# Optimization experiments

Hardware: AMD Instinct MI355X
Metric: run time of the kernel (lower is better)

Reference implementation:

```python
import jax, jax.numpy as jnp
import numpy as np

B, T, IN, H = 512, 512, 1, 64


def _lstm_dir(x, w_ih, w_hh, b_ih, b_hh, reverse):
    """Single-direction LSTM over x:[B,T,D]. PyTorch gate order i,f,g,o."""
    # Precompute input contribution for all timesteps (one big GEMM).
    xg = jnp.einsum('btd,gd->btg', x, w_ih) + (b_ih + b_hh)  # [B,T,4H]
    if reverse:
        xg = xg[:, ::-1]
    Hh = w_hh.shape[1]
    w_hh_t = w_hh.T  # [H,4H]

    def step(carry, g_t):
        h, c = carry
        g = g_t + h @ w_hh_t  # [B,4H]
        i, f, gc, o = jnp.split(g, 4, axis=-1)
        c = jax.nn.sigmoid(f) * c + jax.nn.sigmoid(i) * jnp.tanh(gc)
        h = jax.nn.sigmoid(o) * jnp.tanh(c)
        return (h, c), h

    b = x.shape[0]
    init = (jnp.zeros((b, Hh), x.dtype), jnp.zeros((b, Hh), x.dtype))
    _, hs = jax.lax.scan(step, init, jnp.swapaxes(xg, 0, 1))  # hs:[T,B,H]
    hs = jnp.swapaxes(hs, 0, 1)  # [B,T,H]
    return hs[:, ::-1] if reverse else hs


def _bilstm_layer(x, wf, rf, bf, bf2, wr, rr, br, br2):
    fwd = _lstm_dir(x, wf, rf, bf, bf2, reverse=False)
    bwd = _lstm_dir(x, wr, rr, br, br2, reverse=True)
    return jnp.concatenate([fwd, bwd], axis=-1)  # [B,T,2H]


def setup_inputs() -> dict:
    key = jax.random.key(0)
    ks = jax.random.split(key, 20)
    s = 1.0 / np.sqrt(H)
    u = lambda k, shape: jax.random.uniform(k, shape, jnp.float32, -s, s)
    inp = {'x': jax.random.normal(ks[0], (B, T, IN), jnp.float32)}
    # layer 0 (input dim IN), layer 1 (input dim 2H), fwd and reverse dirs
    inp['w_ih_l0'] = u(ks[1], (4 * H, IN)); inp['w_hh_l0'] = u(ks[2], (4 * H, H))
    inp['b_ih_l0'] = u(ks[3], (4 * H,));   inp['b_hh_l0'] = u(ks[4], (4 * H,))
    inp['w_ih_l0r'] = u(ks[5], (4 * H, IN)); inp['w_hh_l0r'] = u(ks[6], (4 * H, H))
    inp['b_ih_l0r'] = u(ks[7], (4 * H,));    inp['b_hh_l0r'] = u(ks[8], (4 * H,))
    inp['w_ih_l1'] = u(ks[9], (4 * H, 2 * H)); inp['w_hh_l1'] = u(ks[10], (4 * H, H))
    inp['b_ih_l1'] = u(ks[11], (4 * H,));      inp['b_hh_l1'] = u(ks[12], (4 * H,))
    inp['w_ih_l1r'] = u(ks[13], (4 * H, 2 * H)); inp['w_hh_l1r'] = u(ks[14], (4 * H, H))
    inp['b_ih_l1r'] = u(ks[15], (4 * H,));       inp['b_hh_l1r'] = u(ks[16], (4 * H,))
    inp['fc_w'] = u(ks[17], (1, 2 * H)); inp['fc_b'] = u(ks[18], (1,))
    return inp


def reference(x, w_ih_l0, w_hh_l0, b_ih_l0, b_hh_l0,
              w_ih_l0r, w_hh_l0r, b_ih_l0r, b_hh_l0r,
              w_ih_l1, w_hh_l1, b_ih_l1, b_hh_l1,
              w_ih_l1r, w_hh_l1r, b_ih_l1r, b_hh_l1r,
              fc_w, fc_b):
    h0 = _bilstm_layer(x, w_ih_l0, w_hh_l0, b_ih_l0, b_hh_l0,
                       w_ih_l0r, w_hh_l0r, b_ih_l0r, b_hh_l0r)
    h1 = _bilstm_layer(h0, w_ih_l1, w_hh_l1, b_ih_l1, b_hh_l1,
                       w_ih_l1r, w_hh_l1r, b_ih_l1r, b_hh_l1r)
    last = h1[:, -1, :]  # [B,2H]
    return last @ fc_w.T + fc_b  # [B,1]
```

## Files before the change

### kernel.cpp

```cpp
#include <hip/hip_runtime.h>
#include <cstddef>
#include <cstdint>

#define Tn 512
#define Bn 512

__device__ __forceinline__ float rlane(float v, int lane) {
    return __uint_as_float((unsigned)__builtin_amdgcn_readlane((int)__float_as_uint(v), lane));
}
__device__ __forceinline__ float sigm(float x) { return 1.0f / (1.0f + __expf(-x)); }
__device__ __forceinline__ float tanhf_(float x) { return 1.0f - 2.0f / (1.0f + __expf(2.0f * x)); }

#define BAR_LGKM() asm volatile("s_waitcnt lgkmcnt(0)\n\ts_barrier" ::: "memory")

__global__ __launch_bounds__(512, 2) void k_lstm_l0(
    const float* __restrict__ x,
    const float* __restrict__ wih_f, const float* __restrict__ whh_f,
    const float* __restrict__ bih_f, const float* __restrict__ bhh_f,
    const float* __restrict__ wih_r, const float* __restrict__ whh_r,
    const float* __restrict__ bih_r, const float* __restrict__ bhh_r,
    float* __restrict__ h0)
{
    const int tid = threadIdx.x;
    const int ti  = tid >> 7;
    const int kh  = (tid >> 6) & 1;
    const int j   = tid & 63;
    const int e   = ti >> 1;
    const int dir = ti & 1;
    const int b   = blockIdx.x * 2 + e;
    const int klo = kh * 32;

    const float* __restrict__ wih = dir ? wih_r : wih_f;
    const float* __restrict__ whh = dir ? whh_r : whh_f;
    const float* __restrict__ bih = dir ? bih_r : bih_f;
    const float* __restrict__ bhh = dir ? bhh_r : bhh_f;

    __shared__ float  xs[2][Tn];
    __shared__ float4 part[4][2][2][64];

    xs[0][tid] = x[(size_t)(blockIdx.x * 2 + 0) * Tn + tid];
    xs[1][tid] = x[(size_t)(blockIdx.x * 2 + 1) * Tn + tid];

    float wt[4][32];
    float wx[4], bias[4];
    #pragma unroll
    for (int g = 0; g < 4; ++g) {
        const int r = g * 64 + j;
        wx[g]   = wih[r];
        bias[g] = bih[r] + bhh[r];
        const float* __restrict__ ws = whh + (size_t)r * 64 + klo;
        #pragma unroll
        for (int k4 = 0; k4 < 8; ++k4) {
            const float4 w4 = *reinterpret_cast<const float4*>(ws + k4 * 4);
            wt[g][k4 * 4 + 0] = w4.x; wt[g][k4 * 4 + 1] = w4.y;
            wt[g][k4 * 4 + 2] = w4.z; wt[g][k4 * 4 + 3] = w4.w;
        }
    }
    __syncthreads();

    float h = 0.0f, c = 0.0f;
    float* __restrict__ outp = h0 + (size_t)b * Tn * 128 + dir * 64 + j;

    for (int s = 0; s < Tn; ++s) {
        const int t  = dir ? (Tn - 1 - s) : s;
        const int bf = s & 1;
        const float xt = xs[e][t];

        float a0 = 0.0f, a1 = 0.0f, a2 = 0.0f, a3 = 0.0f;
        #pragma unroll
        for (int kk = 0; kk < 32; ++kk) {
            const float hk = rlane(h, klo + kk);
            a0 = fmaf(hk, wt[0][kk], a0);
            a1 = fmaf(hk, wt[1][kk], a1);
            a2 = fmaf(hk, wt[2][kk], a2);
            a3 = fmaf(hk, wt[3][kk], a3);
        }
        part[ti][bf][kh][j] = make_float4(a0, a1, a2, a3);
        BAR_LGKM();
        const float4 pA = part[ti][bf][0][j];
        const float4 pB = part[ti][bf][1][j];
        const float gi = fmaf(xt, wx[0], bias[0]) + pA.x + pB.x;
        const float gf = fmaf(xt, wx[1], bias[1]) + pA.y + pB.y;
        const float gg = fmaf(xt, wx[2], bias[2]) + pA.z + pB.z;
        const float go = fmaf(xt, wx[3], bias[3]) + pA.w + pB.w;
        c = sigm(gf) * c + sigm(gi) * tanhf_(gg);
        h = sigm(go) * tanhf_(c);
        if (kh == 0) outp[(size_t)t * 128] = h;
    }
}

__global__ __launch_bounds__(512, 2) void k_lstm_l1f(
    const float* __restrict__ h0,
    const float* __restrict__ wih, const float* __restrict__ whh,
    const float* __restrict__ bih, const float* __restrict__ bhh,
    float* __restrict__ h1last)
{
    const int tid = threadIdx.x;
    const int e   = tid >> 8;
    const int wv  = (tid >> 6) & 3;
    const int j   = tid & 63;
    const int b   = blockIdx.x * 2 + e;
    const int kbase = wv * 48;

    __shared__ float4 part[2][2][4][64];

    float wt[4][48];
    float bias[4];
    #pragma unroll
    for (int g = 0; g < 4; ++g) {
        const int r = g * 64 + j;
        bias[g] = bih[r] + bhh[r];
        #pragma unroll
        for (int k4 = 0; k4 < 12; ++k4) {
            const int k = kbase + k4 * 4;
            const float* __restrict__ src = (k < 128)
                ? (wih + (size_t)r * 128 + k)
                : (whh + (size_t)r * 64 + (k - 128));
            const float4 w4 = *reinterpret_cast<const float4*>(src);
            wt[g][k4 * 4 + 0] = w4.x; wt[g][k4 * 4 + 1] = w4.y;
            wt[g][k4 * 4 + 2] = w4.z; wt[g][k4 * 4 + 3] = w4.w;
        }
    }

    const float* __restrict__ xrow = h0 + (size_t)b * Tn * 128;

    float x1a = 0.0f, x1b = 0.0f;
    if (wv <= 1) x1a = xrow[j];
    if (wv == 1 || wv == 2) x1b = xrow[64 + j];
    float h = 0.0f, c = 0.0f;

    for (int t = 0; t < Tn; ++t) {
        const int bf = t & 1;
        const int tn = (t + 1 < Tn) ? (t + 1) : t;
        float nx1a = 0.0f, nx1b = 0.0f;
        if (wv <= 1)            nx1a = xrow[(size_t)tn * 128 + j];
        if (wv == 1 || wv == 2) nx1b = xrow[(size_t)tn * 128 + 64 + j];

        float a0 = 0.0f, a1 = 0.0f, a2 = 0.0f, a3 = 0.0f;
        if (wv == 0) {
            #pragma unroll
            for (int kk = 0; kk < 48; ++kk) {
                const float v = rlane(x1a, kk);
                a0 = fmaf(v, wt[0][kk], a0); a1 = fmaf(v, wt[1][kk], a1);
                a2 = fmaf(v, wt[2][kk], a2); a3 = fmaf(v, wt[3][kk], a3);
            }
        } else if (wv == 1) {
            #pragma unroll
            for (int kk = 0; kk < 48; ++kk) {
                const float v = (kk < 16) ? rlane(x1a, 48 + kk) : rlane(x1b, kk - 16);
                a0 = fmaf(v, wt[0][kk], a0); a1 = fmaf(v, wt[1][kk], a1);
                a2 = fmaf(v, wt[2][kk], a2); a3 = fmaf(v, wt[3][kk], a3);
            }
        } else if (wv == 2) {
            #pragma unroll
            for (int kk = 0; kk < 48; ++kk) {
                const float v = (kk < 32) ? rlane(x1b, 32 + kk) : rlane(h, kk - 32);
                a0 = fmaf(v, wt[0][kk], a0); a1 = fmaf(v, wt[1][kk], a1);
                a2 = fmaf(v, wt[2][kk], a2); a3 = fmaf(v, wt[3][kk], a3);
            }
        } else {
            #pragma unroll
            for (int kk = 0; kk < 48; ++kk) {
                const float v = rlane(h, 16 + kk);
                a0 = fmaf(v, wt[0][kk], a0); a1 = fmaf(v, wt[1][kk], a1);
                a2 = fmaf(v, wt[2][kk], a2); a3 = fmaf(v, wt[3][kk], a3);
            }
        }
        part[e][bf][wv][j] = make_float4(a0, a1, a2, a3);
        BAR_LGKM();
        if (wv >= 2) {
            const float4 q0 = part[e][bf][0][j];
            const float4 q1 = part[e][bf][1][j];
            const float4 q2 = part[e][bf][2][j];
            const float4 q3 = part[e][bf][3][j];
            const float gi = bias[0] + q0.x + q1.x + q2.x + q3.x;
            const float gf = bias[1] + q0.y + q1.y + q2.y + q3.y;
            const float gg = bias[2] + q0.z + q1.z + q2.z + q3.z;
            const float go = bias[3] + q0.w + q1.w + q2.w + q3.w;
            c = sigm(gf) * c + sigm(gi) * tanhf_(gg);
            h = sigm(go) * tanhf_(c);
        }
        x1a = nx1a; x1b = nx1b;
    }
    if (wv == 2) h1last[(size_t)b * 64 + j] = h;
}

__global__ __launch_bounds__(64, 1) void k_l1r_fc(
    const float* __restrict__ h0,
    const float* __restrict__ wihr,
    const float* __restrict__ bihr, const float* __restrict__ bhhr,
    const float* __restrict__ h1last,
    const float* __restrict__ fcw, const float* __restrict__ fcb,
    float* __restrict__ out)
{
    const int b = blockIdx.x;
    const int j = threadIdx.x;
    const float* __restrict__ xrow = h0 + ((size_t)b * Tn + (Tn - 1)) * 128;
    const float x1a = xrow[j];
    const float x1b = xrow[64 + j];
    float acc[4];
    #pragma unroll
    for (int g = 0; g < 4; ++g) {
        const int r = g * 64 + j;
        float a = bihr[r] + bhhr[r];
        const float* __restrict__ wr = wihr + (size_t)r * 128;
        #pragma unroll
        for (int d4 = 0; d4 < 16; ++d4) {
            const float4 w4 = *reinterpret_cast<const float4*>(&wr[d4 * 4]);
            a = fmaf(rlane(x1a, d4 * 4 + 0), w4.x, a);
            a = fmaf(rlane(x1a, d4 * 4 + 1), w4.y, a);
            a = fmaf(rlane(x1a, d4 * 4 + 2), w4.z, a);
            a = fmaf(rlane(x1a, d4 * 4 + 3), w4.w, a);
        }
        #pragma unroll
        for (int d4 = 0; d4 < 16; ++d4) {
            const float4 w4 = *reinterpret_cast<const float4*>(&wr[64 + d4 * 4]);
            a = fmaf(rlane(x1b, d4 * 4 + 0), w4.x, a);
            a = fmaf(rlane(x1b, d4 * 4 + 1), w4.y, a);
            a = fmaf(rlane(x1b, d4 * 4 + 2), w4.z, a);
            a = fmaf(rlane(x1b, d4 * 4 + 3), w4.w, a);
        }
        acc[g] = a;
    }
    const float cr = sigm(acc[0]) * tanhf_(acc[2]);
    const float hr = sigm(acc[3]) * tanhf_(cr);
    float v = h1last[(size_t)b * 64 + j] * fcw[j] + hr * fcw[64 + j];
    #pragma unroll
    for (int off = 32; off > 0; off >>= 1) v += __shfl_xor(v, off, 64);
    if (j == 0) out[b] = v + fcb[0];
}

extern "C" void kernel_launch(void* const* d_in, const int* in_sizes, int n_in,
                              void* d_out, int out_size, void* d_ws, size_t ws_size,
                              hipStream_t stream)
{
    const float* x       = (const float*)d_in[0];
    const float* wih_l0  = (const float*)d_in[1];
    const float* whh_l0  = (const float*)d_in[2];
    const float* bih_l0  = (const float*)d_in[3];
    const float* bhh_l0  = (const float*)d_in[4];
    const float* wih_l0r = (const float*)d_in[5];
    const float* whh_l0r = (const float*)d_in[6];
    const float* bih_l0r = (const float*)d_in[7];
    const float* bhh_l0r = (const float*)d_in[8];
    const float* wih_l1  = (const float*)d_in[9];
    const float* whh_l1  = (const float*)d_in[10];
    const float* bih_l1  = (const float*)d_in[11];
    const float* bhh_l1  = (const float*)d_in[12];
    const float* wih_l1r = (const float*)d_in[13];
    const float* whh_l1r = (const float*)d_in[14];
    const float* bih_l1r = (const float*)d_in[15];
    const float* bhh_l1r = (const float*)d_in[16];
    const float* fcw     = (const float*)d_in[17];
    const float* fcb     = (const float*)d_in[18];
    (void)whh_l1r; (void)in_sizes; (void)n_in; (void)out_size;

    float* h0     = (float*)d_ws;
    float* h1last = h0 + (size_t)Bn * Tn * 128;
    (void)ws_size;

    k_lstm_l0<<<dim3(Bn / 2), dim3(512), 0, stream>>>(
        x, wih_l0, whh_l0, bih_l0, bhh_l0,
        wih_l0r, whh_l0r, bih_l0r, bhh_l0r, h0);
    k_lstm_l1f<<<dim3(Bn / 2), dim3(512), 0, stream>>>(
        h0, wih_l1, whh_l1, bih_l1, bhh_l1, h1last);
    k_l1r_fc<<<dim3(Bn), dim3(64), 0, stream>>>(
        h0, wih_l1r, bih_l1r, bhh_l1r, h1last, fcw, fcb, (float*)d_out);
}
```

Measured before the change: 1.172 ms.

## Restructure layer-0 LSTM into one block per sequence-direction with packed FMA dot products

Layer-0 kernel now launches one 128-thread block per (batch, direction) instead of a 512-thread block covering two sequences and both directions. Each wave now owns two gates over the full K=64 using packed f32x2 FMAs, replacing the previous K-split across two waves, and the two waves exchange gate pairs through shared memory. The goal is to shorten each step's serial critical path, use packed FMA throughput, and spread work over more, smaller blocks. The cost is 64 readlanes per step per wave instead of 32, and more weight registers per thread. The layer-1 changes are minor reorders plus keeping the old value when a prefetch is skipped.

```diff
diff --git a/kernel.cpp b/kernel.cpp
--- a/kernel.cpp
+++ b/kernel.cpp
@@ -5,6 +5,8 @@
 #define Tn 512
 #define Bn 512
 
+typedef float f32x2 __attribute__((ext_vector_type(2)));
+
 __device__ __forceinline__ float rlane(float v, int lane) {
     return __uint_as_float((unsigned)__builtin_amdgcn_readlane((int)__float_as_uint(v), lane));
 }
@@ -13,79 +15,81 @@
 
 #define BAR_LGKM() asm volatile("s_waitcnt lgkmcnt(0)\n\ts_barrier" ::: "memory")
 
-__global__ __launch_bounds__(512, 2) void k_lstm_l0(
+#define DOTP(SRC, G)                                                         \
+    do {                                                                     \
+        f32x2 _qa = {0.f, 0.f}, _qb = {0.f, 0.f};                            \
+        _Pragma("unroll")                                                    \
+        for (int _k = 0; _k < 64; _k += 2) {                                 \
+            const float _v0 = rlane((SRC), _k);                              \
+            const float _v1 = rlane((SRC), _k + 1);                          \
+            _qa = __builtin_elementwise_fma((f32x2){_v0, _v0}, w2[_k], _qa); \
+            _qb = __builtin_elementwise_fma((f32x2){_v1, _v1}, w2[_k + 1], _qb); \
+        }                                                                    \
+        (G) += _qa + _qb;                                                    \
+    } while (0)
+
+#define ACT_PAIR(P, O, C, H)                                   \
+    do {                                                       \
+        const float _gi = gp ? (O).x : (P).x;                  \
+        const float _gf = gp ? (O).y : (P).y;                  \
+        const float _gg = gp ? (P).x : (O).x;                  \
+        const float _go = gp ? (P).y : (O).y;                  \
+        (C) = sigm(_gf) * (C) + sigm(_gi) * tanhf_(_gg);       \
+        (H) = sigm(_go) * tanhf_(C);                           \
+    } while (0)
+
+__global__ __launch_bounds__(128, 2) void k_lstm_l0(
     const float* __restrict__ x,
     const float* __restrict__ wih_f, const float* __restrict__ whh_f,
     const float* __restrict__ bih_f, const float* __restrict__ bhh_f,
     const float* __restrict__ wih_r, const float* __restrict__ whh_r,
     const float* __restrict__ bih_r, const float* __restrict__ bhh_r,
-    float* __restrict__ h0)
+    float* __restrict__ h0out)
 {
     const int tid = threadIdx.x;
-    const int ti  = tid >> 7;
-    const int kh  = (tid >> 6) & 1;
+    const int gp  = tid >> 6;
     const int j   = tid & 63;
-    const int e   = ti >> 1;
-    const int dir = ti & 1;
-    const int b   = blockIdx.x * 2 + e;
-    const int klo = kh * 32;
+    const int b   = blockIdx.x >> 1;
+    const int dir = blockIdx.x & 1;
 
     const float* __restrict__ wih = dir ? wih_r : wih_f;
     const float* __restrict__ whh = dir ? whh_r : whh_f;
     const float* __restrict__ bih = dir ? bih_r : bih_f;
     const float* __restrict__ bhh = dir ? bhh_r : bhh_f;
 
-    __shared__ float  xs[2][Tn];
-    __shared__ float4 part[4][2][2][64];
-
-    xs[0][tid] = x[(size_t)(blockIdx.x * 2 + 0) * Tn + tid];
-    xs[1][tid] = x[(size_t)(blockIdx.x * 2 + 1) * Tn + tid];
-
-    float wt[4][32];
-    float wx[4], bias[4];
-    #pragma unroll
-    for (int g = 0; g < 4; ++g) {
-        const int r = g * 64 + j;
-        wx[g]   = wih[r];
-        bias[g] = bih[r] + bhh[r];
-        const float* __restrict__ ws = whh + (size_t)r * 64 + klo;
-        #pragma unroll
-        for (int k4 = 0; k4 < 8; ++k4) {
-            const float4 w4 = *reinterpret_cast<const float4*>(ws + k4 * 4);
-            wt[g][k4 * 4 + 0] = w4.x; wt[g][k4 * 4 + 1] = w4.y;
-            wt[g][k4 * 4 + 2] = w4.z; wt[g][k4 * 4 + 3] = w4.w;
-        }
-    }
+    __shared__ float xs[Tn];
+    __shared__ f32x2 pp[2][2][64];
+
+    #pragma unroll
+    for (int i = 0; i < Tn / 128; ++i)
+        xs[i * 128 + tid] = x[(size_t)b * Tn + i * 128 + tid];
+
+    const int r0 = gp * 128 + j;
+    const int r1 = gp * 128 + 64 + j;
+    f32x2 w2[64];
+    #pragma unroll
+    for (int k = 0; k < 64; ++k)
+        w2[k] = (f32x2){whh[(size_t)r0 * 64 + k], whh[(size_t)r1 * 64 + k]};
+    const f32x2 wx   = {wih[r0], wih[r1]};
+    const f32x2 bias = {bih[r0] + bhh[r0], bih[r1] + bhh[r1]};
+
     __syncthreads();
 
-    float h = 0.0f, c = 0.0f;
-    float* __restrict__ outp = h0 + (size_t)b * Tn * 128 + dir * 64 + j;
+    float h = 0.f, c = 0.f;
+    float* __restrict__ outp = h0out + (size_t)b * Tn * 128 + dir * 64 + j;
 
     for (int s = 0; s < Tn; ++s) {
         const int t  = dir ? (Tn - 1 - s) : s;
         const int bf = s & 1;
-        const float xt = xs[e][t];
-
-        float a0 = 0.0f, a1 = 0.0f, a2 = 0.0f, a3 = 0.0f;
-        #pragma unroll
-        for (int kk = 0; kk < 32; ++kk) {
-            const float hk = rlane(h, klo + kk);
-            a0 = fmaf(hk, wt[0][kk], a0);
-            a1 = fmaf(hk, wt[1][kk], a1);
-            a2 = fmaf(hk, wt[2][kk], a2);
-            a3 = fmaf(hk, wt[3][kk], a3);
-        }
-        part[ti][bf][kh][j] = make_float4(a0, a1, a2, a3);
+        const float xt = xs[t];
+
+        f32x2 p = __builtin_elementwise_fma((f32x2){xt, xt}, wx, bias);
+        DOTP(h, p);
+        pp[bf][gp][j] = p;
         BAR_LGKM();
-        const float4 pA = part[ti][bf][0][j];
-        const float4 pB = part[ti][bf][1][j];
-        const float gi = fmaf(xt, wx[0], bias[0]) + pA.x + pB.x;
-        const float gf = fmaf(xt, wx[1], bias[1]) + pA.y + pB.y;
-        const float gg = fmaf(xt, wx[2], bias[2]) + pA.z + pB.z;
-        const float go = fmaf(xt, wx[3], bias[3]) + pA.w + pB.w;
-        c = sigm(gf) * c + sigm(gi) * tanhf_(gg);
-        h = sigm(go) * tanhf_(c);
-        if (kh == 0) outp[(size_t)t * 128] = h;
+        const f32x2 o = pp[bf][1 ^ gp][j];
+        ACT_PAIR(p, o, c, h);
+        if (gp == 0) outp[(size_t)t * 128] = h;
     }
 }
 
@@ -104,12 +108,17 @@
 
     __shared__ float4 part[2][2][4][64];
 
-    float wt[4][48];
     float bias[4];
     #pragma unroll
     for (int g = 0; g < 4; ++g) {
         const int r = g * 64 + j;
         bias[g] = bih[r] + bhh[r];
+    }
+
+    float wt[4][48];
+    #pragma unroll
+    for (int g = 0; g < 4; ++g) {
+        const int r = g * 64 + j;
         #pragma unroll
         for (int k4 = 0; k4 < 12; ++k4) {
             const int k = kbase + k4 * 4;
@@ -132,7 +141,7 @@
     for (int t = 0; t < Tn; ++t) {
         const int bf = t & 1;
         const int tn = (t + 1 < Tn) ? (t + 1) : t;
-        float nx1a = 0.0f, nx1b = 0.0f;
+        float nx1a = x1a, nx1b = x1b;
         if (wv <= 1)            nx1a = xrow[(size_t)tn * 128 + j];
         if (wv == 1 || wv == 2) nx1b = xrow[(size_t)tn * 128 + 64 + j];
 
@@ -186,7 +195,7 @@
 }
 
 __global__ __launch_bounds__(64, 1) void k_l1r_fc(
-    const float* __restrict__ h0,
+    const float* __restrict__ h0in,
     const float* __restrict__ wihr,
     const float* __restrict__ bihr, const float* __restrict__ bhhr,
     const float* __restrict__ h1last,
@@ -195,7 +204,7 @@
 {
     const int b = blockIdx.x;
     const int j = threadIdx.x;
-    const float* __restrict__ xrow = h0 + ((size_t)b * Tn + (Tn - 1)) * 128;
+    const float* __restrict__ xrow = h0in + ((size_t)b * Tn + (Tn - 1)) * 128;
     const float x1a = xrow[j];
     const float x1b = xrow[64 + j];
     float acc[4];
@@ -253,13 +262,12 @@
     const float* bhh_l1r = (const float*)d_in[16];
     const float* fcw     = (const float*)d_in[17];
     const float* fcb     = (const float*)d_in[18];
-    (void)whh_l1r; (void)in_sizes; (void)n_in; (void)out_size;
+    (void)whh_l1r; (void)in_sizes; (void)n_in; (void)out_size; (void)ws_size;
 
     float* h0     = (float*)d_ws;
     float* h1last = h0 + (size_t)Bn * Tn * 128;
-    (void)ws_size;
-
-    k_lstm_l0<<<dim3(Bn / 2), dim3(512), 0, stream>>>(
+
+    k_lstm_l0<<<dim3(Bn * 2), dim3(128), 0, stream>>>(
         x, wih_l0, whh_l0, bih_l0, bhh_l0,
         wih_l0r, whh_l0r, bih_l0r, bhh_l0r, h0);
     k_lstm_l1f<<<dim3(Bn / 2), dim3(512), 0, stream>>>(
```

New measurement: 1.278 ms. +9.0%, slower.

## Restructure layer-0 LSTM to one wave per direction handling two batch rows

Applied to the files above, without the earlier changes.

The layer-0 kernel moves from 512-thread blocks, where two half-K waves per (row, direction) combine partial sums through LDS and a barrier every step, to single-wave blocks. Each wave computes the full 64-wide recurrent dot product for two batch rows and broadcasts h with readlane. This removes the per-step barrier and LDS reduction and gives each shared weight read two FMAs. In exchange each lane holds 256 weight registers, which raises register pressure, and the serial per-step FMA chain doubles in length. The layer-1 edits are small reorderings of the bias loads and of the prefetch defaults.

```diff
diff --git a/kernel.cpp b/kernel.cpp
--- a/kernel.cpp
+++ b/kernel.cpp
@@ -13,79 +13,80 @@
 
 #define BAR_LGKM() asm volatile("s_waitcnt lgkmcnt(0)\n\ts_barrier" ::: "memory")
 
-__global__ __launch_bounds__(512, 2) void k_lstm_l0(
+__global__ __launch_bounds__(64, 1) void k_lstm_l0(
     const float* __restrict__ x,
     const float* __restrict__ wih_f, const float* __restrict__ whh_f,
     const float* __restrict__ bih_f, const float* __restrict__ bhh_f,
     const float* __restrict__ wih_r, const float* __restrict__ whh_r,
     const float* __restrict__ bih_r, const float* __restrict__ bhh_r,
-    float* __restrict__ h0)
-{
-    const int tid = threadIdx.x;
-    const int ti  = tid >> 7;
-    const int kh  = (tid >> 6) & 1;
-    const int j   = tid & 63;
-    const int e   = ti >> 1;
-    const int dir = ti & 1;
-    const int b   = blockIdx.x * 2 + e;
-    const int klo = kh * 32;
+    float* __restrict__ h0out)
+{
+    const int j   = threadIdx.x;
+    const int bp  = blockIdx.x >> 1;
+    const int dir = blockIdx.x & 1;
+    const int b0  = bp * 2;
+    const int b1  = b0 + 1;
 
     const float* __restrict__ wih = dir ? wih_r : wih_f;
     const float* __restrict__ whh = dir ? whh_r : whh_f;
     const float* __restrict__ bih = dir ? bih_r : bih_f;
     const float* __restrict__ bhh = dir ? bhh_r : bhh_f;
 
-    __shared__ float  xs[2][Tn];
-    __shared__ float4 part[4][2][2][64];
-
-    xs[0][tid] = x[(size_t)(blockIdx.x * 2 + 0) * Tn + tid];
-    xs[1][tid] = x[(size_t)(blockIdx.x * 2 + 1) * Tn + tid];
-
-    float wt[4][32];
+    __shared__ float xs[2][Tn];
+    #pragma unroll
+    for (int i = 0; i < Tn / 64; ++i) {
+        xs[0][i * 64 + j] = x[(size_t)b0 * Tn + i * 64 + j];
+        xs[1][i * 64 + j] = x[(size_t)b1 * Tn + i * 64 + j];
+    }
+
+    float w[4][64];
     float wx[4], bias[4];
     #pragma unroll
     for (int g = 0; g < 4; ++g) {
         const int r = g * 64 + j;
         wx[g]   = wih[r];
         bias[g] = bih[r] + bhh[r];
-        const float* __restrict__ ws = whh + (size_t)r * 64 + klo;
-        #pragma unroll
-        for (int k4 = 0; k4 < 8; ++k4) {
-            const float4 w4 = *reinterpret_cast<const float4*>(ws + k4 * 4);
-            wt[g][k4 * 4 + 0] = w4.x; wt[g][k4 * 4 + 1] = w4.y;
-            wt[g][k4 * 4 + 2] = w4.z; wt[g][k4 * 4 + 3] = w4.w;
-        }
-    }
-    __syncthreads();
-
-    float h = 0.0f, c = 0.0f;
-    float* __restrict__ outp = h0 + (size_t)b * Tn * 128 + dir * 64 + j;
+        #pragma unroll
+        for (int k4 = 0; k4 < 16; ++k4) {
+            const float4 v = *reinterpret_cast<const float4*>(&whh[(size_t)r * 64 + k4 * 4]);
+            w[g][k4 * 4 + 0] = v.x; w[g][k4 * 4 + 1] = v.y;
+            w[g][k4 * 4 + 2] = v.z; w[g][k4 * 4 + 3] = v.w;
+        }
+    }
+
+    float hA = 0.0f, cA = 0.0f, hB = 0.0f, cB = 0.0f;
+    float* __restrict__ opA = h0out + (size_t)b0 * Tn * 128 + dir * 64 + j;
+    float* __restrict__ opB = h0out + (size_t)b1 * Tn * 128 + dir * 64 + j;
 
     for (int s = 0; s < Tn; ++s) {
-        const int t  = dir ? (Tn - 1 - s) : s;
-        const int bf = s & 1;
-        const float xt = xs[e][t];
-
-        float a0 = 0.0f, a1 = 0.0f, a2 = 0.0f, a3 = 0.0f;
-        #pragma unroll
-        for (int kk = 0; kk < 32; ++kk) {
-            const float hk = rlane(h, klo + kk);
-            a0 = fmaf(hk, wt[0][kk], a0);
-            a1 = fmaf(hk, wt[1][kk], a1);
-            a2 = fmaf(hk, wt[2][kk], a2);
-            a3 = fmaf(hk, wt[3][kk], a3);
-        }
-        part[ti][bf][kh][j] = make_float4(a0, a1, a2, a3);
-        BAR_LGKM();
-        const float4 pA = part[ti][bf][0][j];
-        const float4 pB = part[ti][bf][1][j];
-        const float gi = fmaf(xt, wx[0], bias[0]) + pA.x + pB.x;
-        const float gf = fmaf(xt, wx[1], bias[1]) + pA.y + pB.y;
-        const float gg = fmaf(xt, wx[2], bias[2]) + pA.z + pB.z;
-        const float go = fmaf(xt, wx[3], bias[3]) + pA.w + pB.w;
-        c = sigm(gf) * c + sigm(gi) * tanhf_(gg);
-        h = sigm(go) * tanhf_(c);
-        if (kh == 0) outp[(size_t)t * 128] = h;
+        const int t = dir ? (Tn - 1 - s) : s;
+        const float xtA = xs[0][t];
+        const float xtB = xs[1][t];
+
+        float aA0 = fmaf(xtA, wx[0], bias[0]);
+        float aA1 = fmaf(xtA, wx[1], bias[1]);
+        float aA2 = fmaf(xtA, wx[2], bias[2]);
+        float aA3 = fmaf(xtA, wx[3], bias[3]);
+        float aB0 = fmaf(xtB, wx[0], bias[0]);
+        float aB1 = fmaf(xtB, wx[1], bias[1]);
+        float aB2 = fmaf(xtB, wx[2], bias[2]);
+        float aB3 = fmaf(xtB, wx[3], bias[3]);
+        #pragma unroll
+        for (int k = 0; k < 64; ++k) {
+            const float vA = rlane(hA, k);
+            const float vB = rlane(hB, k);
+            const float w0 = w[0][k], w1 = w[1][k], w2 = w[2][k], w3 = w[3][k];
+            aA0 = fmaf(vA, w0, aA0);  aB0 = fmaf(vB, w0, aB0);
+            aA1 = fmaf(vA, w1, aA1);  aB1 = fmaf(vB, w1, aB1);
+            aA2 = fmaf(vA, w2, aA2);  aB2 = fmaf(vB, w2, aB2);
+            aA3 = fmaf(vA, w3, aA3);  aB3 = fmaf(vB, w3, aB3);
+        }
+        cA = sigm(aA1) * cA + sigm(aA0) * tanhf_(aA2);
+        hA = sigm(aA3) * tanhf_(cA);
+        cB = sigm(aB1) * cB + sigm(aB0) * tanhf_(aB2);
+        hB = sigm(aB3) * tanhf_(cB);
+        opA[(size_t)t * 128] = hA;
+        opB[(size_t)t * 128] = hB;
     }
 }
 
@@ -104,12 +105,17 @@
 
     __shared__ float4 part[2][2][4][64];
 
+    float bias[4];
+    #pragma unroll
+    for (int g = 0; g < 4; ++g) {
+        const int r = g * 64 + j;
+        bias[g] = bih[r] + bhh[r];
+    }
+
     float wt[4][48];
-    float bias[4];
-    #pragma unroll
-    for (int g = 0; g < 4; ++g) {
-        const int r = g * 64 + j;
-        bias[g] = bih[r] + bhh[r];
+    #pragma unroll
+    for (int g = 0; g < 4; ++g) {
+        const int r = g * 64 + j;
         #pragma unroll
         for (int k4 = 0; k4 < 12; ++k4) {
             const int k = kbase + k4 * 4;
@@ -132,7 +138,7 @@
     for (int t = 0; t < Tn; ++t) {
         const int bf = t & 1;
         const int tn = (t + 1 < Tn) ? (t + 1) : t;
-        float nx1a = 0.0f, nx1b = 0.0f;
+        float nx1a = x1a, nx1b = x1b;
         if (wv <= 1)            nx1a = xrow[(size_t)tn * 128 + j];
         if (wv == 1 || wv == 2) nx1b = xrow[(size_t)tn * 128 + 64 + j];
 
@@ -186,7 +192,7 @@
 }
 
 __global__ __launch_bounds__(64, 1) void k_l1r_fc(
-    const float* __restrict__ h0,
+    const float* __restrict__ h0in,
     const float* __restrict__ wihr,
     const float* __restrict__ bihr, const float* __restrict__ bhhr,
     const float* __restrict__ h1last,
@@ -195,7 +201,7 @@
 {
     const int b = blockIdx.x;
     const int j = threadIdx.x;
-    const float* __restrict__ xrow = h0 + ((size_t)b * Tn + (Tn - 1)) * 128;
+    const float* __restrict__ xrow = h0in + ((size_t)b * Tn + (Tn - 1)) * 128;
     const float x1a = xrow[j];
     const float x1b = xrow[64 + j];
     float acc[4];
@@ -253,13 +259,12 @@
     const float* bhh_l1r = (const float*)d_in[16];
     const float* fcw     = (const float*)d_in[17];
     const float* fcb     = (const float*)d_in[18];
-    (void)whh_l1r; (void)in_sizes; (void)n_in; (void)out_size;
+    (void)whh_l1r; (void)in_sizes; (void)n_in; (void)out_size; (void)ws_size;
 
     float* h0     = (float*)d_ws;
     float* h1last = h0 + (size_t)Bn * Tn * 128;
-    (void)ws_size;
-
-    k_lstm_l0<<<dim3(Bn / 2), dim3(512), 0, stream>>>(
+
+    k_lstm_l0<<<dim3(Bn), dim3(64), 0, stream>>>(
         x, wih_l0, whh_l0, bih_l0, bhh_l0,
         wih_l0r, whh_l0r, bih_l0r, bhh_l0r, h0);
     k_lstm_l1f<<<dim3(Bn / 2), dim3(512), 0, stream>>>(
```

After: 1.373 ms. 1.17x slower.
